# Optimization experiments

Measured on AMD Instinct MI355X. Metric: run time of the kernel, lower is better.

## Reference

```python
import jax, jax.numpy as jnp
import numpy as np

TEMPERATURE = 0.5
EPS = 1e-8  # matches torch CosineSimilarity eps


def setup_inputs() -> dict:
    key = jax.random.key(0)
    k1, k2 = jax.random.split(key)
    N, D = 4096, 256
    z1 = jax.random.normal(k1, (N, D), dtype=jnp.float32)
    z2 = jax.random.normal(k2, (N, D), dtype=jnp.float32)
    return {"z1": z1, "z2": z2}


def reference(z1, z2):
    N = z1.shape[0]
    z = jnp.concatenate([z1, z2], axis=0)            # [2N, D]
    norm = jnp.linalg.norm(z, axis=-1, keepdims=True)
    zn = z / jnp.maximum(norm, EPS)                  # L2-normalized
    sim = (zn @ zn.T) / TEMPERATURE                  # [2N, 2N] cosine sim / temp
    # mask self-similarity on the diagonal
    diag = jnp.eye(2 * N, dtype=bool)
    sim = jnp.where(diag, -jnp.inf, sim)
    # positive pair labels: row i pairs with i+N (first half) or i-N (second half)
    labels = jnp.concatenate([jnp.arange(N) + N, jnp.arange(N)])
    logp = jax.nn.log_softmax(sim, axis=-1)
    loss = -jnp.mean(logp[jnp.arange(2 * N), labels])
    return loss
```

## Files before the change

### kernel.cpp

```cpp
#include <hip/hip_runtime.h>
#include <hip/hip_bf16.h>


#define NROWS 8192
#define NHALF 4096
#define DDIM  256
#define NSTRIP 32
#define TILE  256

typedef __bf16 bf16;
typedef __bf16 bf16x4 __attribute__((ext_vector_type(4)));
typedef __bf16 bf16x8 __attribute__((ext_vector_type(8)));
typedef float  f32x4  __attribute__((ext_vector_type(4)));

__constant__ const float kSqrtC = 1.69864359f;
__constant__ const float kLn2   = 0.6931471805599453f;

__device__ __forceinline__ void load_lds16(const bf16* g, bf16* l) {
  __builtin_amdgcn_global_load_lds(
      (const __attribute__((address_space(1))) unsigned int*)g,
      (__attribute__((address_space(3))) unsigned int*)l, 16, 0, 0);
}

__global__ void k_normalize(const float* __restrict__ z1, const float* __restrict__ z2,
                            bf16* __restrict__ zn, float* __restrict__ rowsum,
                            float* __restrict__ out) {
  const int wave = threadIdx.x >> 6, lane = threadIdx.x & 63;
  const int row = blockIdx.x * 4 + wave;
  const float* src = (row < NHALF) ? z1 + (size_t)row * DDIM
                                   : z2 + (size_t)(row - NHALF) * DDIM;
  f32x4 v = *(const f32x4*)(src + lane * 4);
  float ss = v.x * v.x + v.y * v.y + v.z * v.z + v.w * v.w;
#pragma unroll
  for (int off = 1; off < 64; off <<= 1) ss += __shfl_xor(ss, off);
  const float inv = kSqrtC / fmaxf(sqrtf(ss), 1e-8f);
  bf16x4 o;
  o.x = (bf16)(v.x * inv); o.y = (bf16)(v.y * inv);
  o.z = (bf16)(v.z * inv); o.w = (bf16)(v.w * inv);
  *(bf16x4*)(zn + (size_t)row * DDIM + lane * 4) = o;
  if (lane == 0) rowsum[row] = 0.0f;
  if (blockIdx.x == 0 && threadIdx.x == 0) out[0] = 0.0f;
}

__global__ __launch_bounds__(512, 2) void k_gram(const bf16* __restrict__ zn,
                                                 float* __restrict__ rowsum) {
  __shared__ __align__(16) bf16 bstage[32 * 512];
  __shared__ float colsum[320];
  const int tid  = threadIdx.x;
  const int wave = tid >> 6, lane = tid & 63;
  const int quad = lane >> 4, l15 = lane & 15;

  int t0, cnt;
  if (blockIdx.x < 64) { t0 = blockIdx.x * 5; cnt = 5; }
  else                 { t0 = 320 + ((int)blockIdx.x - 64) * 4; cnt = 4; }

  int R = 0, rem = t0;
  while (rem >= 4 * (NSTRIP - R)) { rem -= 4 * (NSTRIP - R); ++R; }
  int cloc = rem;

  for (int i = tid; i < 320; i += 512) colsum[i] = 0.0f;

  bf16x8 a[2][8];
  auto loadA = [&](int Rv) {
#pragma unroll
    for (int s = 0; s < 2; ++s) {
      const int row = Rv * TILE + wave * 32 + s * 16 + l15;
      const bf16x8* ap = (const bf16x8*)(zn + (size_t)row * DDIM);
#pragma unroll
      for (int k = 0; k < 8; ++k) a[s][k] = ap[k * 4 + quad];
    }
  };
  loadA(R);

  float sum[2][4] = {{0.f, 0.f, 0.f, 0.f}, {0.f, 0.f, 0.f, 0.f}};

  auto flush_rows = [&]() {
#pragma unroll
    for (int s = 0; s < 2; ++s)
#pragma unroll
      for (int r = 0; r < 4; ++r) {
        float v = sum[s][r];
        v += __shfl_xor(v, 1); v += __shfl_xor(v, 2);
        v += __shfl_xor(v, 4); v += __shfl_xor(v, 8);
        if (l15 == 0)
          atomicAdd(&rowsum[R * TILE + wave * 32 + s * 16 + quad * 4 + r], v);
        sum[s][r] = 0.0f;
      }
  };

  const f32x4 zero4 = {0.f, 0.f, 0.f, 0.f};

  for (int tl = 0; tl < cnt; ++tl) {
    const int colbase = R * TILE + cloc * 64;
    const bool dt = (cloc < 4);

    __syncthreads();
#pragma unroll
    for (int c = 0; c < 4; ++c) {
      const int chunk = wave * 4 + c;
      const int kk = chunk >> 2, cs = chunk & 3;
      const bf16* g = zn + (size_t)(colbase + cs * 16 + l15) * DDIM + kk * 32 + quad * 8;
      load_lds16(g, &bstage[chunk * 512]);
    }
    __syncthreads();

    f32x4 acc[2][4];
#pragma unroll
    for (int k = 0; k < 8; ++k) {
      bf16x8 b[4];
#pragma unroll
      for (int cs = 0; cs < 4; ++cs)
        b[cs] = *(const bf16x8*)(&bstage[(k * 4 + cs) * 512 + lane * 8]);
#pragma unroll
      for (int s = 0; s < 2; ++s)
#pragma unroll
        for (int cs = 0; cs < 4; ++cs)
          acc[s][cs] = __builtin_amdgcn_mfma_f32_16x16x32_bf16(
              a[s][k], b[cs], k ? acc[s][cs] : zero4, 0, 0, 0);
    }

#pragma unroll
    for (int cs = 0; cs < 4; ++cs) {
      float cp = 0.0f;
#pragma unroll
      for (int s = 0; s < 2; ++s)
#pragma unroll
        for (int r = 0; r < 4; ++r) {
          const float v = __builtin_amdgcn_exp2f(acc[s][cs][r]);
          sum[s][r] += v;
          cp += v;
        }
      if (!dt) {
        cp += __shfl_xor(cp, 16);
        cp += __shfl_xor(cp, 32);
        if (lane < 16) atomicAdd(&colsum[tl * 64 + cs * 16 + l15], cp);
      }
    }

    ++cloc;
    if (cloc == 4 * (NSTRIP - R) && tl + 1 < cnt) {
      flush_rows();
      ++R; cloc = 0;
      loadA(R);
    }
  }
  flush_rows();

  __syncthreads();
  for (int idx = tid; idx < cnt * 64; idx += 512) {
    const int tloc = idx >> 6;
    int Rv = 0, r2 = t0 + tloc;
    while (r2 >= 4 * (NSTRIP - Rv)) { r2 -= 4 * (NSTRIP - Rv); ++Rv; }
    const int col = Rv * TILE + r2 * 64 + (idx & 63);
    atomicAdd(&rowsum[col], colsum[idx]);
  }
}

__device__ __forceinline__ float dot4(bf16x4 a, bf16x4 b) {
  return (float)a.x * (float)b.x + (float)a.y * (float)b.y +
         (float)a.z * (float)b.z + (float)a.w * (float)b.w;
}

__global__ void k_finalize(const bf16* __restrict__ zn, const float* __restrict__ rowsum,
                           float* __restrict__ out) {
  const int wave = threadIdx.x >> 6, lane = threadIdx.x & 63;
  const int gw = blockIdx.x * 4 + wave;
  float acc = 0.0f;
  for (int t = 0; t < 16; ++t) {
    const int q = gw * 16 + t, pq = q + NHALF;
    bf16x4 zq = *(const bf16x4*)(zn + (size_t)q  * DDIM + lane * 4);
    bf16x4 zp = *(const bf16x4*)(zn + (size_t)pq * DDIM + lane * 4);
    float dqq = dot4(zq, zq);
    float dpp = dot4(zp, zp);
    float dqp = dot4(zq, zp);
#pragma unroll
    for (int off = 1; off < 64; off <<= 1) {
      dqq += __shfl_xor(dqq, off);
      dpp += __shfl_xor(dpp, off);
      dqp += __shfl_xor(dqp, off);
    }
    if (lane == 0) {
      const float lseq = __builtin_amdgcn_logf(rowsum[q]  - __builtin_amdgcn_exp2f(dqq)) * kLn2;
      const float lsep = __builtin_amdgcn_logf(rowsum[pq] - __builtin_amdgcn_exp2f(dpp)) * kLn2;
      acc += lseq + lsep - 2.0f * dqp * kLn2;
    }
  }
  __shared__ float ws4[4];
  if (lane == 0) ws4[wave] = acc;
  __syncthreads();
  if (threadIdx.x == 0)
    atomicAdd(out, (ws4[0] + ws4[1] + ws4[2] + ws4[3]) * (1.0f / (float)NROWS));
}

extern "C" void kernel_launch(void* const* d_in, const int* in_sizes, int n_in,
                              void* d_out, int out_size, void* d_ws, size_t ws_size,
                              hipStream_t stream) {
  const float* z1 = (const float*)d_in[0];
  const float* z2 = (const float*)d_in[1];
  unsigned char* ws = (unsigned char*)d_ws;

  bf16* zn = (bf16*)ws;
  float* rowsum = (float*)(ws + (size_t)NROWS * DDIM * sizeof(bf16));
  float* out = (float*)d_out;

  hipLaunchKernelGGL(k_normalize, dim3(NROWS / 4), dim3(256), 0, stream, z1, z2, zn, rowsum, out);
  hipLaunchKernelGGL(k_gram, dim3(512), dim3(512), 0, stream, zn, rowsum);
  hipLaunchKernelGGL(k_finalize, dim3(64), dim3(256), 0, stream, zn, rowsum, out);
}
```

Before: 115.1 us.

## Double-buffer B tiles via register prefetch and halve gram grid

The direct global-to-LDS loads of each B tile are replaced by a register prefetch of the next tile, issued before the MFMA loop and written into the other of two padded LDS buffers after it, so only one barrier per iteration is needed. The grid shrinks from 512 to 256 blocks, with each block processing 8-9 tiles instead of 4-5. The LDS row stride is padded to avoid bank conflicts. The intent is to hide global load latency behind compute, at the cost of more registers and fewer blocks in flight.

```diff
diff --git a/kernel.cpp b/kernel.cpp
--- a/kernel.cpp
+++ b/kernel.cpp
@@ -7,6 +7,9 @@
 #define DDIM  256
 #define NSTRIP 32
 #define TILE  256
+#define BN    64
+#define LDSB  528
+#define MAXIT 9
 
 typedef __bf16 bf16;
 typedef __bf16 bf16x4 __attribute__((ext_vector_type(4)));
@@ -15,12 +18,6 @@
 
 __constant__ const float kSqrtC = 1.69864359f;
 __constant__ const float kLn2   = 0.6931471805599453f;
-
-__device__ __forceinline__ void load_lds16(const bf16* g, bf16* l) {
-  __builtin_amdgcn_global_load_lds(
-      (const __attribute__((address_space(1))) unsigned int*)g,
-      (__attribute__((address_space(3))) unsigned int*)l, 16, 0, 0);
-}
 
 __global__ void k_normalize(const float* __restrict__ z1, const float* __restrict__ z2,
                             bf16* __restrict__ zn, float* __restrict__ rowsum,
@@ -44,21 +41,21 @@
 
 __global__ __launch_bounds__(512, 2) void k_gram(const bf16* __restrict__ zn,
                                                  float* __restrict__ rowsum) {
-  __shared__ __align__(16) bf16 bstage[32 * 512];
-  __shared__ float colsum[320];
+  __shared__ __align__(16) unsigned char lds[2][BN * LDSB];
+  __shared__ float colsum[MAXIT * BN];
   const int tid  = threadIdx.x;
   const int wave = tid >> 6, lane = tid & 63;
   const int quad = lane >> 4, l15 = lane & 15;
 
   int t0, cnt;
-  if (blockIdx.x < 64) { t0 = blockIdx.x * 5; cnt = 5; }
-  else                 { t0 = 320 + ((int)blockIdx.x - 64) * 4; cnt = 4; }
+  if (blockIdx.x < 64) { t0 = blockIdx.x * 9; cnt = 9; }
+  else                 { t0 = 576 + ((int)blockIdx.x - 64) * 8; cnt = 8; }
 
   int R = 0, rem = t0;
   while (rem >= 4 * (NSTRIP - R)) { rem -= 4 * (NSTRIP - R); ++R; }
   int cloc = rem;
 
-  for (int i = tid; i < 320; i += 512) colsum[i] = 0.0f;
+  for (int i = tid; i < MAXIT * BN; i += 512) colsum[i] = 0.0f;
 
   bf16x8 a[2][8];
   auto loadA = [&](int Rv) {
@@ -73,7 +70,6 @@
   loadA(R);
 
   float sum[2][4] = {{0.f, 0.f, 0.f, 0.f}, {0.f, 0.f, 0.f, 0.f}};
-
   auto flush_rows = [&]() {
 #pragma unroll
     for (int s = 0; s < 2; ++s)
@@ -88,21 +84,34 @@
       }
   };
 
+  const int tr = tid >> 3, tc = tid & 7;
+  uint4 g[4];
+  auto prefetch = [&](int colbase) {
+    const unsigned char* gp = (const unsigned char*)(zn + (size_t)(colbase + tr) * DDIM);
+#pragma unroll
+    for (int j = 0; j < 4; ++j) g[j] = *(const uint4*)(gp + (tc + 8 * j) * 16);
+  };
+  auto commit = [&](int buf) {
+#pragma unroll
+    for (int j = 0; j < 4; ++j)
+      *(uint4*)(&lds[buf][tr * LDSB + (tc + 8 * j) * 16]) = g[j];
+  };
+
+  prefetch(R * TILE + cloc * 64);
+  commit(0);
+
   const f32x4 zero4 = {0.f, 0.f, 0.f, 0.f};
 
   for (int tl = 0; tl < cnt; ++tl) {
-    const int colbase = R * TILE + cloc * 64;
+    __syncthreads();
+    const int cur = tl & 1;
     const bool dt = (cloc < 4);
 
-    __syncthreads();
-#pragma unroll
-    for (int c = 0; c < 4; ++c) {
-      const int chunk = wave * 4 + c;
-      const int kk = chunk >> 2, cs = chunk & 3;
-      const bf16* g = zn + (size_t)(colbase + cs * 16 + l15) * DDIM + kk * 32 + quad * 8;
-      load_lds16(g, &bstage[chunk * 512]);
-    }
-    __syncthreads();
+    if (tl + 1 < cnt) {
+      int Rn = R, cn = cloc + 1;
+      if (cn == 4 * (NSTRIP - Rn)) { cn = 0; ++Rn; }
+      prefetch(Rn * TILE + cn * 64);
+    }
 
     f32x4 acc[2][4];
 #pragma unroll
@@ -110,7 +119,7 @@
       bf16x8 b[4];
 #pragma unroll
       for (int cs = 0; cs < 4; ++cs)
-        b[cs] = *(const bf16x8*)(&bstage[(k * 4 + cs) * 512 + lane * 8]);
+        b[cs] = *(const bf16x8*)(&lds[cur][(cs * 16 + l15) * LDSB + k * 64 + quad * 16]);
 #pragma unroll
       for (int s = 0; s < 2; ++s)
 #pragma unroll
@@ -118,6 +127,8 @@
           acc[s][cs] = __builtin_amdgcn_mfma_f32_16x16x32_bf16(
               a[s][k], b[cs], k ? acc[s][cs] : zero4, 0, 0, 0);
     }
+
+    if (tl + 1 < cnt) commit(cur ^ 1);
 
 #pragma unroll
     for (int cs = 0; cs < 4; ++cs) {
@@ -204,6 +215,6 @@
   float* out = (float*)d_out;
 
   hipLaunchKernelGGL(k_normalize, dim3(NROWS / 4), dim3(256), 0, stream, z1, z2, zn, rowsum, out);
-  hipLaunchKernelGGL(k_gram, dim3(512), dim3(512), 0, stream, zn, rowsum);
+  hipLaunchKernelGGL(k_gram, dim3(256), dim3(512), 0, stream, zn, rowsum);
   hipLaunchKernelGGL(k_finalize, dim3(64), dim3(256), 0, stream, zn, rowsum, out);
 }
```

After: 117.5 us. 1.02x slower.
